# Kernel tuning notes

Measured on AMD Instinct MI355X. Metric: run time of the kernel, lower is better.

Reference implementation:

```python
import jax, jax.numpy as jnp
import numpy as np

N_EMBD = 1024
N_HEAD = 16
HEAD_DIM = N_EMBD // N_HEAD
INNER = 4 * N_EMBD
EPS = 1e-5


def setup_inputs() -> dict:
    key = jax.random.key(0)
    ks = jax.random.split(key, 13)
    s = lambda d: 1.0 / np.sqrt(d)
    return {
        "x": jax.random.normal(ks[0], (2, 2048, N_EMBD), jnp.float32),
        "ln1_g": jnp.ones((N_EMBD,), jnp.float32),
        "ln1_b": jnp.zeros((N_EMBD,), jnp.float32),
        "w_attn": jax.random.normal(ks[1], (N_EMBD, 3 * N_EMBD), jnp.float32) * s(N_EMBD),
        "b_attn": jnp.zeros((3 * N_EMBD,), jnp.float32),
        "w_proj": jax.random.normal(ks[2], (N_EMBD, N_EMBD), jnp.float32) * s(N_EMBD),
        "b_proj": jnp.zeros((N_EMBD,), jnp.float32),
        "ln2_g": jnp.ones((N_EMBD,), jnp.float32),
        "ln2_b": jnp.zeros((N_EMBD,), jnp.float32),
        "w_fc": jax.random.normal(ks[3], (N_EMBD, INNER), jnp.float32) * s(N_EMBD),
        "b_fc": jnp.zeros((INNER,), jnp.float32),
        "w_fc2": jax.random.normal(ks[4], (INNER, N_EMBD), jnp.float32) * s(INNER),
        "b_fc2": jnpp if False else jnp.zeros((N_EMBD,), jnp.float32),
    }


def _layernorm(x, g, b):
    mu = jnp.mean(x, axis=-1, keepdims=True)
    var = jnp.mean(jnp.square(x - mu), axis=-1, keepdims=True)
    return (x - mu) * jax.lax.rsqrt(var + EPS) * g + b


def _attention(x, w_attn, b_attn, w_proj, b_proj):
    B, T, C = x.shape
    qkv = x @ w_attn + b_attn                      # [B,T,3C]
    q, k, v = jnp.split(qkv, 3, axis=-1)
    q = q.reshape(B, T, N_HEAD, HEAD_DIM).transpose(0, 2, 1, 3)  # [B,H,T,D]
    k = k.reshape(B, T, N_HEAD, HEAD_DIM).transpose(0, 2, 1, 3)
    v = v.reshape(B, T, N_HEAD, HEAD_DIM).transpose(0, 2, 1, 3)
    scale = HEAD_DIM ** -0.5
    scores = jnp.einsum("bhqd,bhkd->bhqk", q, k) * scale         # [B,H,T,T]
    causal = jnp.triu(jnp.ones((T, T), jnp.bool_), k=1)
    scores = jnp.where(causal, -jnp.inf, scores)
    attn = jax.nn.softmax(scores, axis=-1)
    out = jnp.einsum("bhqk,bhkd->bhqd", attn, v)                 # [B,H,T,D]
    out = out.transpose(0, 2, 1, 3).reshape(B, T, C)
    return out @ w_proj + b_proj


def reference(x, ln1_g, ln1_b, w_attn, b_attn, w_proj, b_proj,
              ln2_g, ln2_b, w_fc, b_fc, w_fc2, b_fc2):
    h = x + _attention(_layernorm(x, ln1_g, ln1_b), w_attn, b_attn, w_proj, b_proj)
    m = _layernorm(h, ln2_g, ln2_b)
    m = jax.nn.gelu(m @ w_fc + b_fc, approximate=False) @ w_fc2 + b_fc2
    return h + m
```

## Files before the change

### kernel.cpp

```cpp
#include <hip/hip_runtime.h>

typedef unsigned short u16;
typedef unsigned int u32;
typedef short v8s __attribute__((ext_vector_type(8)));
typedef short v4s __attribute__((ext_vector_type(4)));
typedef float v4f __attribute__((ext_vector_type(4)));

__device__ __forceinline__ float b2f(u16 v) {
    return __uint_as_float(((u32)v) << 16);
}
__device__ __forceinline__ u16 f2b(float f) {
    u32 u = __float_as_uint(f);
    return (u16)((u + 0x7FFFu + ((u >> 16) & 1u)) >> 16);
}

__device__ __forceinline__ void gload_lds16(const u16* g, u16* l) {
    __builtin_amdgcn_global_load_lds((const __attribute__((address_space(1))) void*)g,
                                     (__attribute__((address_space(3))) void*)l, 16, 0, 0);
}

__global__ void detect_k(const void* x, int* flag) {
    __shared__ int cnt;
    if (threadIdx.x == 0) cnt = 0;
    __syncthreads();
    const u16* p = (const u16*)x;
    int bad = 0;
    for (int i = threadIdx.x; i < 4096; i += 256) {
        int e = (p[i] >> 7) & 0xFF;
        if (e != 0 && (e < 100 || e > 140)) bad++;
    }
    atomicAdd(&cnt, bad);
    __syncthreads();
    if (threadIdx.x == 0) *flag = (cnt > 256) ? 1 : 0;
}

__global__ void cvt_k(const void* __restrict__ src, u16* __restrict__ dst, int n,
                      const int* __restrict__ flag) {
    const int isf32 = *flag;
    for (int i = blockIdx.x * 256 + threadIdx.x; i < n; i += gridDim.x * 256)
        dst[i] = isf32 ? f2b(((const float*)src)[i]) : ((const u16*)src)[i];
}

struct P8 { const void* p[8]; };
__global__ void cvt_small_k(P8 src, u16* __restrict__ bb, const int* __restrict__ flag) {
    const int isf32 = *flag;
    const int len[8] = {3072, 1024, 4096, 1024, 1024, 1024, 1024, 1024};
    const int doff[8] = {0, 4096, 8192, 12288, 16384, 17408, 18432, 19456};
    int gi = blockIdx.x * 256 + threadIdx.x;
    int seg = 0, off = gi;
    while (seg < 7 && off >= len[seg]) { off -= len[seg]; seg++; }
    if (off < len[seg]) {
        const void* s = src.p[seg];
        bb[doff[seg] + off] = isf32 ? f2b(((const float*)s)[off]) : ((const u16*)s)[off];
    }
}

__global__ void transpose_k(const void* __restrict__ in, u16* __restrict__ out, int R, int C,
                            const int* __restrict__ flag) {
    __shared__ u16 t[32][33];
    const int isf32 = *flag;
    const int c0 = blockIdx.x * 32, r0 = blockIdx.y * 32;
    for (int i = threadIdx.y; i < 32; i += 8) {
        size_t idx = (size_t)(r0 + i) * C + c0 + threadIdx.x;
        t[i][threadIdx.x] = isf32 ? f2b(((const float*)in)[idx]) : ((const u16*)in)[idx];
    }
    __syncthreads();
    for (int i = threadIdx.y; i < 32; i += 8)
        out[(size_t)(c0 + i) * R + r0 + threadIdx.x] = t[threadIdx.x][i];
}

__global__ __launch_bounds__(256) void layernorm_k(const u16* __restrict__ x,
                                                   const u16* __restrict__ g,
                                                   const u16* __restrict__ bta,
                                                   u16* __restrict__ out) {
    const int wid = threadIdx.x >> 6, lane = threadIdx.x & 63;
    const size_t row = (size_t)blockIdx.x * 4 + wid;
    const u16* xr = x + row * 1024 + lane * 16;
    u16 v[16];
    *(uint4*)&v[0] = *(const uint4*)xr;
    *(uint4*)&v[8] = *(const uint4*)(xr + 8);
    float f[16], s = 0.f, sq = 0.f;
#pragma unroll
    for (int i = 0; i < 16; i++) { f[i] = b2f(v[i]); s += f[i]; sq += f[i] * f[i]; }
#pragma unroll
    for (int d = 1; d < 64; d <<= 1) { s += __shfl_xor(s, d, 64); sq += __shfl_xor(sq, d, 64); }
    const float mean = s * (1.f / 1024.f);
    const float var = sq * (1.f / 1024.f) - mean * mean;
    const float rstd = rsqrtf(var + 1e-5f);
    u16 gv[16], bv[16];
    *(uint4*)&gv[0] = *(const uint4*)(g + lane * 16);
    *(uint4*)&gv[8] = *(const uint4*)(g + lane * 16 + 8);
    *(uint4*)&bv[0] = *(const uint4*)(bta + lane * 16);
    *(uint4*)&bv[8] = *(const uint4*)(bta + lane * 16 + 8);
    u16 ov[16];
#pragma unroll
    for (int i = 0; i < 16; i++) ov[i] = f2b((f[i] - mean) * rstd * b2f(gv[i]) + b2f(bv[i]));
    u16* orow = out + row * 1024 + lane * 16;
    *(uint4*)orow = *(uint4*)&ov[0];
    *(uint4*)(orow + 8) = *(uint4*)&ov[8];
}

__global__ __launch_bounds__(256) void gemm_bt_k(const u16* __restrict__ A,
                                                 const u16* __restrict__ Bt,
                                                 const u16* __restrict__ bias,
                                                 const u16* __restrict__ res,
                                                 void* __restrict__ C,
                                                 int M, int N, int K, int do_gelu,
                                                 const int* __restrict__ outf32) {
    __shared__ __align__(16) u16 As[2][4096];
    __shared__ __align__(16) u16 Bs[2][4096];
    const int tid = threadIdx.x;
    const int wid = tid >> 6, lane = tid & 63;
    const int lg = lane >> 4, lm = lane & 15;
    const int wr = wid >> 1, wc = wid & 1;
    const int m0 = blockIdx.y * 128, n0 = blockIdx.x * 128;

    const v4f vzero = {0.f, 0.f, 0.f, 0.f};
    v4f acc[4][4];
#pragma unroll
    for (int i = 0; i < 4; i++)
#pragma unroll
        for (int j = 0; j < 4; j++) acc[i][j] = vzero;

    const int srow = tid >> 2;
    const int scol = (tid & 3) * 8;
    const u16* Ag = A + (size_t)(m0 + srow) * K + scol;
    const u16* Bg = Bt + (size_t)(n0 + srow) * K + scol;

    const int nt = K >> 5;
    {
        gload_lds16(Ag, &As[0][0] + wid * 512);
        gload_lds16(Ag + (size_t)64 * K, &As[0][2048] + wid * 512);
        gload_lds16(Bg, &Bs[0][0] + wid * 512);
        gload_lds16(Bg + (size_t)64 * K, &Bs[0][2048] + wid * 512);
    }
    for (int t = 0; t < nt; ++t) {
        const int cur = t & 1;
        if (t + 1 < nt) {
            const int k1 = (t + 1) << 5;
            gload_lds16(Ag + k1, &As[cur ^ 1][0] + wid * 512);
            gload_lds16(Ag + (size_t)64 * K + k1, &As[cur ^ 1][2048] + wid * 512);
            gload_lds16(Bg + k1, &Bs[cur ^ 1][0] + wid * 512);
            gload_lds16(Bg + (size_t)64 * K + k1, &Bs[cur ^ 1][2048] + wid * 512);
            asm volatile("s_waitcnt vmcnt(4)" ::: "memory");
        } else {
            asm volatile("s_waitcnt vmcnt(0)" ::: "memory");
        }
        __builtin_amdgcn_s_barrier();
        v8s af[4], bf[4];
#pragma unroll
        for (int i = 0; i < 4; i++)
            af[i] = *(const v8s*)&As[cur][(wr * 64 + i * 16 + lm) * 32 + lg * 8];
#pragma unroll
        for (int j = 0; j < 4; j++)
            bf[j] = *(const v8s*)&Bs[cur][(wc * 64 + j * 16 + lm) * 32 + lg * 8];
#pragma unroll
        for (int i = 0; i < 4; i++)
#pragma unroll
            for (int j = 0; j < 4; j++)
                acc[i][j] = __builtin_amdgcn_mfma_f32_16x16x32_bf16(af[i], bf[j], acc[i][j], 0, 0, 0);
        asm volatile("s_waitcnt lgkmcnt(0)" ::: "memory");
        __builtin_amdgcn_sched_barrier(0);
        __builtin_amdgcn_s_barrier();
    }

    const int of32 = outf32 ? *outf32 : 0;
#pragma unroll
    for (int i = 0; i < 4; i++) {
#pragma unroll
        for (int r = 0; r < 4; r++) {
            const int row = m0 + wr * 64 + i * 16 + lg * 4 + r;
            const size_t rb = (size_t)row * N;
#pragma unroll
            for (int j = 0; j < 4; j++) {
                const int col = n0 + wc * 64 + j * 16 + lm;
                float v = acc[i][j][r] + b2f(bias[col]);
                if (do_gelu) v = 0.5f * v * (1.0f + erff(v * 0.70710678118f));
                if (res) v += b2f(res[rb + col]);
                if (of32) ((float*)C)[rb + col] = v;
                else ((u16*)C)[rb + col] = f2b(v);
            }
        }
    }
}

__global__ __launch_bounds__(256) void gemm_qkv_k(const u16* __restrict__ A,
                                                  const u16* __restrict__ Bt,
                                                  const u16* __restrict__ bias,
                                                  u16* __restrict__ Qh,
                                                  u16* __restrict__ Kh,
                                                  u16* __restrict__ Vth) {
    __shared__ __align__(16) u16 As[2][4096];
    __shared__ __align__(16) u16 Bs[2][4096];
    const int tid = threadIdx.x;
    const int wid = tid >> 6, lane = tid & 63;
    const int lg = lane >> 4, lm = lane & 15;
    const int wr = wid >> 1, wc = wid & 1;
    const int m0 = blockIdx.y * 128, n0 = blockIdx.x * 128;
    const int K = 1024;

    const v4f vzero = {0.f, 0.f, 0.f, 0.f};
    v4f acc[4][4];
#pragma unroll
    for (int i = 0; i < 4; i++)
#pragma unroll
        for (int j = 0; j < 4; j++) acc[i][j] = vzero;

    const int srow = tid >> 2;
    const int scol = (tid & 3) * 8;
    const u16* Ag = A + (size_t)(m0 + srow) * K + scol;
    const u16* Bg = Bt + (size_t)(n0 + srow) * K + scol;

    const int nt = K >> 5;
    {
        gload_lds16(Ag, &As[0][0] + wid * 512);
        gload_lds16(Ag + (size_t)64 * K, &As[0][2048] + wid * 512);
        gload_lds16(Bg, &Bs[0][0] + wid * 512);
        gload_lds16(Bg + (size_t)64 * K, &Bs[0][2048] + wid * 512);
    }
    for (int t = 0; t < nt; ++t) {
        const int cur = t & 1;
        if (t + 1 < nt) {
            const int k1 = (t + 1) << 5;
            gload_lds16(Ag + k1, &As[cur ^ 1][0] + wid * 512);
            gload_lds16(Ag + (size_t)64 * K + k1, &As[cur ^ 1][2048] + wid * 512);
            gload_lds16(Bg + k1, &Bs[cur ^ 1][0] + wid * 512);
            gload_lds16(Bg + (size_t)64 * K + k1, &Bs[cur ^ 1][2048] + wid * 512);
            asm volatile("s_waitcnt vmcnt(4)" ::: "memory");
        } else {
            asm volatile("s_waitcnt vmcnt(0)" ::: "memory");
        }
        __builtin_amdgcn_s_barrier();
        v8s af[4], bf[4];
#pragma unroll
        for (int i = 0; i < 4; i++)
            af[i] = *(const v8s*)&As[cur][(wr * 64 + i * 16 + lm) * 32 + lg * 8];
#pragma unroll
        for (int j = 0; j < 4; j++)
            bf[j] = *(const v8s*)&Bs[cur][(wc * 64 + j * 16 + lm) * 32 + lg * 8];
#pragma unroll
        for (int i = 0; i < 4; i++)
#pragma unroll
            for (int j = 0; j < 4; j++)
                acc[i][j] = __builtin_amdgcn_mfma_f32_16x16x32_bf16(af[i], bf[j], acc[i][j], 0, 0, 0);
        asm volatile("s_waitcnt lgkmcnt(0)" ::: "memory");
        __builtin_amdgcn_sched_barrier(0);
        __builtin_amdgcn_s_barrier();
    }

    const int which = n0 >> 10;
    const int h = ((n0 & 1023) >> 6) + wc;
    if (which < 2) {
        u16* dst = which ? Kh : Qh;
        const float qsc = which ? 1.0f : 0.18033688011f;
#pragma unroll
        for (int i = 0; i < 4; i++) {
#pragma unroll
            for (int r = 0; r < 4; r++) {
                const int row = m0 + wr * 64 + i * 16 + lg * 4 + r;
                const int b = row >> 11, t = row & 2047;
                const size_t rb = ((size_t)(b * 16 + h) * 2048 + t) * 64;
#pragma unroll
                for (int j = 0; j < 4; j++) {
                    float v = (acc[i][j][r] + b2f(bias[n0 + wc * 64 + j * 16 + lm])) * qsc;
                    dst[rb + j * 16 + lm] = f2b(v);
                }
            }
        }
    } else {
#pragma unroll
        for (int i = 0; i < 4; i++) {
            const int t0 = m0 + wr * 64 + i * 16 + lg * 4;
            const int b = t0 >> 11, tt = t0 & 2047;
            const int w = tt & 31;
            const int pos = (tt & ~31) + ((w & 15) >> 2) * 8 + ((w >> 4) & 1) * 4;
#pragma unroll
            for (int j = 0; j < 4; j++) {
                const int d = j * 16 + lm;
                const float bv_ = b2f(bias[n0 + wc * 64 + j * 16 + lm]);
                u16 pk[4];
#pragma unroll
                for (int r = 0; r < 4; r++) pk[r] = f2b(acc[i][j][r] + bv_);
                *(v4s*)&Vth[((size_t)(b * 16 + h) * 64 + d) * 2048 + pos] = *(const v4s*)pk;
            }
        }
    }
}

__global__ __launch_bounds__(256, 4) void attn10_k(const u16* __restrict__ Qh,
                                                   const u16* __restrict__ Kh,
                                                   const u16* __restrict__ Vth,
                                                   u16* __restrict__ out) {
    __shared__ __align__(16) u16 Ks[2][4096];
    __shared__ __align__(16) u16 Vs[2][4096];
    const int tid = threadIdx.x;
    const int wid = tid >> 6, lane = tid & 63;
    const int lg = lane >> 4, lm = lane & 15;
    const int i = blockIdx.x;
    const int q = i >> 8, s = i & 255;
    const int bh = s & 31;
    const int g8 = s >> 5;
    const int g = (q == 0) ? g8 : (q == 1) ? (15 - g8) : (q == 2) ? (16 + g8) : (31 - g8);
    const int q0 = g * 64 + wid * 16;
    const int qrow_l = q0 + lm;
    const size_t qkb = (size_t)bh * 2048;
    const v4f vzero = {0.f, 0.f, 0.f, 0.f};
    const int nch = g + 1;

    const int r0 = tid >> 3;
    const int colp = ((tid & 7) * 16) ^ ((r0 & 7) << 4);
    const u16* Ksrc0 = Kh + (qkb + r0) * 64 + (colp >> 1);
    const u16* Ksrc1 = Ksrc0 + 32 * 64;
    const u16* Vsrc0 = Vth + ((size_t)bh * 64 + r0) * 2048 + (colp >> 1);
    const u16* Vsrc1 = Vsrc0 + (size_t)32 * 2048;
    const int wslot = wid * 512;

    const int xorv = (lm & 7) << 4;
    const int ro1 = (lm * 128 + ((lg * 16) ^ xorv)) >> 1;
    const int ro2 = (lm * 128 + (((lg * 16) + 64) ^ xorv)) >> 1;

    v8s aq[2];
    {
        const u16* qp = Qh + (qkb + q0 + lm) * 64 + lg * 8;
        aq[0] = *(const v8s*)qp;
        aq[1] = *(const v8s*)(qp + 32);
    }
    float l_run = 0.f;
    v4f o[4];
#pragma unroll
    for (int dt = 0; dt < 4; dt++) o[dt] = vzero;

    gload_lds16(Ksrc0, &Ks[0][0] + wslot);
    gload_lds16(Ksrc1, &Ks[0][2048] + wslot);
    gload_lds16(Vsrc0, &Vs[0][0] + wslot);
    gload_lds16(Vsrc1, &Vs[0][2048] + wslot);

    for (int ci = 0; ci < nch; ++ci) {
        const int cur = ci & 1;
        if (ci + 1 < nch) {
            const u16* kc = Ksrc0 + (ci + 1) * 4096;
            const u16* vc = Vsrc0 + (ci + 1) * 64;
            gload_lds16(kc, &Ks[cur ^ 1][0] + wslot);
            gload_lds16(kc + 32 * 64, &Ks[cur ^ 1][2048] + wslot);
            gload_lds16(vc, &Vs[cur ^ 1][0] + wslot);
            gload_lds16(vc + (size_t)32 * 2048, &Vs[cur ^ 1][2048] + wslot);
            asm volatile("s_waitcnt vmcnt(4)" ::: "memory");
        } else {
            asm volatile("s_waitcnt vmcnt(0)" ::: "memory");
        }
        __builtin_amdgcn_s_barrier();

        const u16* KB = &Ks[cur][0];
        const u16* VB = &Vs[cur][0];
        const int k0 = ci << 6;
        v4f sacc[4];
#pragma unroll
        for (int kt = 0; kt < 4; kt++) {
            v8s klo = *(const v8s*)(KB + kt * 1024 + ro1);
            v8s khi = *(const v8s*)(KB + kt * 1024 + ro2);
            sacc[kt] = __builtin_amdgcn_mfma_f32_16x16x32_bf16(klo, aq[0], vzero, 0, 0, 0);
            sacc[kt] = __builtin_amdgcn_mfma_f32_16x16x32_bf16(khi, aq[1], sacc[kt], 0, 0, 0);
        }
        float p[16];
        if (ci == nch - 1) {
#pragma unroll
            for (int kt = 0; kt < 4; kt++)
#pragma unroll
                for (int r = 0; r < 4; r++) {
                    float v = sacc[kt][r];
                    v = (k0 + kt * 16 + lg * 4 + r > qrow_l) ? -200.f : v;
                    p[kt * 4 + r] = exp2f(v);
                }
        } else {
#pragma unroll
            for (int kt = 0; kt < 4; kt++)
#pragma unroll
                for (int r = 0; r < 4; r++) p[kt * 4 + r] = exp2f(sacc[kt][r]);
        }
        float ls = 0.f;
#pragma unroll
        for (int e = 0; e < 16; e++) ls += p[e];
        l_run += ls;
        u32 pk[8];
#pragma unroll
        for (int j = 0; j < 8; j++) {
            u32 lo = __float_as_uint(p[j * 2]) + 0x8000u;
            u32 hi = __float_as_uint(p[j * 2 + 1]) + 0x8000u;
            pk[j] = __builtin_amdgcn_perm(hi, lo, 0x07060302u);
        }
        v8s B0, B1;
        ((u32*)&B0)[0] = pk[0]; ((u32*)&B0)[1] = pk[1];
        ((u32*)&B0)[2] = pk[2]; ((u32*)&B0)[3] = pk[3];
        ((u32*)&B1)[0] = pk[4]; ((u32*)&B1)[1] = pk[5];
        ((u32*)&B1)[2] = pk[6]; ((u32*)&B1)[3] = pk[7];
#pragma unroll
        for (int dt = 0; dt < 4; dt++) {
            v8s vlo = *(const v8s*)(VB + dt * 1024 + ro1);
            v8s vhi = *(const v8s*)(VB + dt * 1024 + ro2);
            o[dt] = __builtin_amdgcn_mfma_f32_16x16x32_bf16(vlo, B0, o[dt], 0, 0, 0);
            o[dt] = __builtin_amdgcn_mfma_f32_16x16x32_bf16(vhi, B1, o[dt], 0, 0, 0);
        }
        asm volatile("s_waitcnt lgkmcnt(0)" ::: "memory");
        __builtin_amdgcn_sched_barrier(0);
        __builtin_amdgcn_s_barrier();
    }
    l_run += __shfl_xor(l_run, 16, 64);
    l_run += __shfl_xor(l_run, 32, 64);
    const int b = bh >> 4, h = bh & 15;
    const float inv = 1.0f / l_run;
    const size_t rowb = ((size_t)b * 2048 + q0 + lm) * 1024 + h * 64;
#pragma unroll
    for (int dt = 0; dt < 4; dt++) {
        u16 pk2[4];
#pragma unroll
        for (int r = 0; r < 4; r++) pk2[r] = f2b(o[dt][r] * inv);
        *(v4s*)&out[rowb + dt * 16 + lg * 4] = *(const v4s*)pk2;
    }
}

extern "C" void kernel_launch(void* const* d_in, const int* in_sizes, int n_in,
                              void* d_out, int out_size, void* d_ws, size_t ws_size,
                              hipStream_t stream) {
    const void* x      = d_in[0];
    const void* ln1_g  = d_in[1];
    const void* ln1_b  = d_in[2];
    const void* w_attn = d_in[3];
    const void* b_attn = d_in[4];
    const void* w_proj = d_in[5];
    const void* b_proj = d_in[6];
    const void* ln2_g  = d_in[7];
    const void* ln2_b  = d_in[8];
    const void* w_fc   = d_in[9];
    const void* b_fc   = d_in[10];
    const void* w_fc2  = d_in[11];
    const void* b_fc2  = d_in[12];

    u16* ws = (u16*)d_ws;
    const size_t Mi = 1u << 20;
    u16* xb       = ws;
    u16* ln_buf   = ws + 4 * Mi;
    u16* h_buf    = ws + 8 * Mi;
    u16* wT_attn  = ws + 12 * Mi;
    u16* wT_proj  = ws + 15 * Mi;
    u16* wT_fc    = ws + 16 * Mi;
    u16* wT_fc2   = ws + 20 * Mi;
    u16* bb       = ws + 24 * Mi;
    u16* bb_attn = bb, *bb_proj = bb + 4096, *bb_fc = bb + 8192, *bb_fc2 = bb + 12288;
    u16* gsmall   = bb + 16384;
    u16* g_ln1g = gsmall, *g_ln1b = gsmall + 1024, *g_ln2g = gsmall + 2048, *g_ln2b = gsmall + 3072;
    int* flag     = (int*)(bb + 24576);
    u16* Qh       = ws + 25 * Mi;
    u16* Kh       = ws + 29 * Mi;
    u16* Vth      = ws + 33 * Mi;
    u16* attn_buf = ws + 37 * Mi;
    u16* fc_buf   = ws + 25 * Mi;

    detect_k<<<1, 256, 0, stream>>>(x, flag);

    cvt_k<<<4096, 256, 0, stream>>>(x, xb, 4 * Mi, flag);
    P8 smalls;
    smalls.p[0] = b_attn; smalls.p[1] = b_proj; smalls.p[2] = b_fc; smalls.p[3] = b_fc2;
    smalls.p[4] = ln1_g;  smalls.p[5] = ln1_b;  smalls.p[6] = ln2_g; smalls.p[7] = ln2_b;
    cvt_small_k<<<52, 256, 0, stream>>>(smalls, bb, flag);

    dim3 tb(32, 8);
    transpose_k<<<dim3(96, 32), tb, 0, stream>>>(w_attn, wT_attn, 1024, 3072, flag);
    transpose_k<<<dim3(32, 32), tb, 0, stream>>>(w_proj, wT_proj, 1024, 1024, flag);
    transpose_k<<<dim3(128, 32), tb, 0, stream>>>(w_fc, wT_fc, 1024, 4096, flag);
    transpose_k<<<dim3(32, 128), tb, 0, stream>>>(w_fc2, wT_fc2, 4096, 1024, flag);

    layernorm_k<<<1024, 256, 0, stream>>>(xb, g_ln1g, g_ln1b, ln_buf);
    gemm_qkv_k<<<dim3(24, 32), 256, 0, stream>>>(ln_buf, wT_attn, bb_attn, Qh, Kh, Vth);
    attn10_k<<<1024, 256, 0, stream>>>(Qh, Kh, Vth, attn_buf);
    gemm_bt_k<<<dim3(8, 32), 256, 0, stream>>>(attn_buf, wT_proj, bb_proj, xb, h_buf,
                                               4096, 1024, 1024, 0, nullptr);
    layernorm_k<<<1024, 256, 0, stream>>>(h_buf, g_ln2g, g_ln2b, ln_buf);
    gemm_bt_k<<<dim3(32, 32), 256, 0, stream>>>(ln_buf, wT_fc, bb_fc, nullptr, fc_buf,
                                                4096, 4096, 1024, 1, nullptr);
    gemm_bt_k<<<dim3(8, 32), 256, 0, stream>>>(fc_buf, wT_fc2, bb_fc2, h_buf, d_out,
                                               4096, 1024, 4096, 0, flag);
}
```

Measured before the change: 462.2 us.

## Triple-buffer GEMM loads, swizzle LDS, remap workgroups, raise MFMA priority

Moves both GEMM kernels from double to triple buffering, issuing loads two K-tiles ahead to hide more global latency. It also applies an XOR swizzle to the LDS layout to cut bank conflicts, remaps workgroup IDs in groups of 8 for better L2 locality, and wraps the MFMA sections of the GEMM and attention kernels in s_setprio. Costs are 1.5x LDS per block, which may lower occupancy, plus the assumption that the grid size divides evenly by 8.

```diff
diff --git a/kernel.cpp b/kernel.cpp
--- a/kernel.cpp
+++ b/kernel.cpp
@@ -100,6 +100,15 @@
     *(uint4*)(orow + 8) = *(uint4*)&ov[8];
 }
 
+#define GEMM_STAGE(tk, buf)                                              \
+    do {                                                                 \
+        const int _k = (tk) << 5;                                        \
+        gload_lds16(Ag + _k, &As[buf][0] + wid * 512);                   \
+        gload_lds16(Ag + (size_t)64 * K + _k, &As[buf][2048] + wid * 512); \
+        gload_lds16(Bg + _k, &Bs[buf][0] + wid * 512);                   \
+        gload_lds16(Bg + (size_t)64 * K + _k, &Bs[buf][2048] + wid * 512); \
+    } while (0)
+
 __global__ __launch_bounds__(256) void gemm_bt_k(const u16* __restrict__ A,
                                                  const u16* __restrict__ Bt,
                                                  const u16* __restrict__ bias,
@@ -107,13 +116,16 @@
                                                  void* __restrict__ C,
                                                  int M, int N, int K, int do_gelu,
                                                  const int* __restrict__ outf32) {
-    __shared__ __align__(16) u16 As[2][4096];
-    __shared__ __align__(16) u16 Bs[2][4096];
+    __shared__ __align__(16) u16 As[3][4096];
+    __shared__ __align__(16) u16 Bs[3][4096];
     const int tid = threadIdx.x;
     const int wid = tid >> 6, lane = tid & 63;
     const int lg = lane >> 4, lm = lane & 15;
     const int wr = wid >> 1, wc = wid & 1;
-    const int m0 = blockIdx.y * 128, n0 = blockIdx.x * 128;
+    const int nwg = gridDim.x * gridDim.y;
+    const int orig = blockIdx.y * gridDim.x + blockIdx.x;
+    const int wg = (orig & 7) * (nwg >> 3) + (orig >> 3);
+    const int m0 = (wg / gridDim.x) * 128, n0 = (wg % gridDim.x) * 128;
 
     const v4f vzero = {0.f, 0.f, 0.f, 0.f};
     v4f acc[4][4];
@@ -123,25 +135,20 @@
         for (int j = 0; j < 4; j++) acc[i][j] = vzero;
 
     const int srow = tid >> 2;
-    const int scol = (tid & 3) * 8;
+    const int scol = (((tid & 3) ^ ((tid >> 3) & 3)) * 8);
     const u16* Ag = A + (size_t)(m0 + srow) * K + scol;
     const u16* Bg = Bt + (size_t)(n0 + srow) * K + scol;
+    const int lgx = (lg ^ ((lm >> 1) & 3)) * 8;
 
     const int nt = K >> 5;
-    {
-        gload_lds16(Ag, &As[0][0] + wid * 512);
-        gload_lds16(Ag + (size_t)64 * K, &As[0][2048] + wid * 512);
-        gload_lds16(Bg, &Bs[0][0] + wid * 512);
-        gload_lds16(Bg + (size_t)64 * K, &Bs[0][2048] + wid * 512);
-    }
+    GEMM_STAGE(0, 0);
+    GEMM_STAGE(1, 1);
     for (int t = 0; t < nt; ++t) {
-        const int cur = t & 1;
-        if (t + 1 < nt) {
-            const int k1 = (t + 1) << 5;
-            gload_lds16(Ag + k1, &As[cur ^ 1][0] + wid * 512);
-            gload_lds16(Ag + (size_t)64 * K + k1, &As[cur ^ 1][2048] + wid * 512);
-            gload_lds16(Bg + k1, &Bs[cur ^ 1][0] + wid * 512);
-            gload_lds16(Bg + (size_t)64 * K + k1, &Bs[cur ^ 1][2048] + wid * 512);
+        const int cur = t % 3;
+        if (t + 2 < nt) {
+            GEMM_STAGE(t + 2, (t + 2) % 3);
+            asm volatile("s_waitcnt vmcnt(8)" ::: "memory");
+        } else if (t + 1 < nt) {
             asm volatile("s_waitcnt vmcnt(4)" ::: "memory");
         } else {
             asm volatile("s_waitcnt vmcnt(0)" ::: "memory");
@@ -150,15 +157,17 @@
         v8s af[4], bf[4];
 #pragma unroll
         for (int i = 0; i < 4; i++)
-            af[i] = *(const v8s*)&As[cur][(wr * 64 + i * 16 + lm) * 32 + lg * 8];
+            af[i] = *(const v8s*)&As[cur][(wr * 64 + i * 16 + lm) * 32 + lgx];
 #pragma unroll
         for (int j = 0; j < 4; j++)
-            bf[j] = *(const v8s*)&Bs[cur][(wc * 64 + j * 16 + lm) * 32 + lg * 8];
+            bf[j] = *(const v8s*)&Bs[cur][(wc * 64 + j * 16 + lm) * 32 + lgx];
+        __builtin_amdgcn_s_setprio(1);
 #pragma unroll
         for (int i = 0; i < 4; i++)
 #pragma unroll
             for (int j = 0; j < 4; j++)
                 acc[i][j] = __builtin_amdgcn_mfma_f32_16x16x32_bf16(af[i], bf[j], acc[i][j], 0, 0, 0);
+        __builtin_amdgcn_s_setprio(0);
         asm volatile("s_waitcnt lgkmcnt(0)" ::: "memory");
         __builtin_amdgcn_sched_barrier(0);
         __builtin_amdgcn_s_barrier();
@@ -190,13 +199,16 @@
                                                   u16* __restrict__ Qh,
                                                   u16* __restrict__ Kh,
                                                   u16* __restrict__ Vth) {
-    __shared__ __align__(16) u16 As[2][4096];
-    __shared__ __align__(16) u16 Bs[2][4096];
+    __shared__ __align__(16) u16 As[3][4096];
+    __shared__ __align__(16) u16 Bs[3][4096];
     const int tid = threadIdx.x;
     const int wid = tid >> 6, lane = tid & 63;
     const int lg = lane >> 4, lm = lane & 15;
     const int wr = wid >> 1, wc = wid & 1;
-    const int m0 = blockIdx.y * 128, n0 = blockIdx.x * 128;
+    const int nwg = gridDim.x * gridDim.y;
+    const int orig = blockIdx.y * gridDim.x + blockIdx.x;
+    const int wg = (orig & 7) * (nwg >> 3) + (orig >> 3);
+    const int m0 = (wg / gridDim.x) * 128, n0 = (wg % gridDim.x) * 128;
     const int K = 1024;
 
     const v4f vzero = {0.f, 0.f, 0.f, 0.f};
@@ -207,25 +219,20 @@
         for (int j = 0; j < 4; j++) acc[i][j] = vzero;
 
     const int srow = tid >> 2;
-    const int scol = (tid & 3) * 8;
+    const int scol = (((tid & 3) ^ ((tid >> 3) & 3)) * 8);
     const u16* Ag = A + (size_t)(m0 + srow) * K + scol;
     const u16* Bg = Bt + (size_t)(n0 + srow) * K + scol;
+    const int lgx = (lg ^ ((lm >> 1) & 3)) * 8;
 
     const int nt = K >> 5;
-    {
-        gload_lds16(Ag, &As[0][0] + wid * 512);
-        gload_lds16(Ag + (size_t)64 * K, &As[0][2048] + wid * 512);
-        gload_lds16(Bg, &Bs[0][0] + wid * 512);
-        gload_lds16(Bg + (size_t)64 * K, &Bs[0][2048] + wid * 512);
-    }
+    GEMM_STAGE(0, 0);
+    GEMM_STAGE(1, 1);
     for (int t = 0; t < nt; ++t) {
-        const int cur = t & 1;
-        if (t + 1 < nt) {
-            const int k1 = (t + 1) << 5;
-            gload_lds16(Ag + k1, &As[cur ^ 1][0] + wid * 512);
-            gload_lds16(Ag + (size_t)64 * K + k1, &As[cur ^ 1][2048] + wid * 512);
-            gload_lds16(Bg + k1, &Bs[cur ^ 1][0] + wid * 512);
-            gload_lds16(Bg + (size_t)64 * K + k1, &Bs[cur ^ 1][2048] + wid * 512);
+        const int cur = t % 3;
+        if (t + 2 < nt) {
+            GEMM_STAGE(t + 2, (t + 2) % 3);
+            asm volatile("s_waitcnt vmcnt(8)" ::: "memory");
+        } else if (t + 1 < nt) {
             asm volatile("s_waitcnt vmcnt(4)" ::: "memory");
         } else {
             asm volatile("s_waitcnt vmcnt(0)" ::: "memory");
@@ -234,15 +241,17 @@
         v8s af[4], bf[4];
 #pragma unroll
         for (int i = 0; i < 4; i++)
-            af[i] = *(const v8s*)&As[cur][(wr * 64 + i * 16 + lm) * 32 + lg * 8];
+            af[i] = *(const v8s*)&As[cur][(wr * 64 + i * 16 + lm) * 32 + lgx];
 #pragma unroll
         for (int j = 0; j < 4; j++)
-            bf[j] = *(const v8s*)&Bs[cur][(wc * 64 + j * 16 + lm) * 32 + lg * 8];
+            bf[j] = *(const v8s*)&Bs[cur][(wc * 64 + j * 16 + lm) * 32 + lgx];
+        __builtin_amdgcn_s_setprio(1);
 #pragma unroll
         for (int i = 0; i < 4; i++)
 #pragma unroll
             for (int j = 0; j < 4; j++)
                 acc[i][j] = __builtin_amdgcn_mfma_f32_16x16x32_bf16(af[i], bf[j], acc[i][j], 0, 0, 0);
+        __builtin_amdgcn_s_setprio(0);
         asm volatile("s_waitcnt lgkmcnt(0)" ::: "memory");
         __builtin_amdgcn_sched_barrier(0);
         __builtin_amdgcn_s_barrier();
@@ -354,6 +363,7 @@
         const u16* VB = &Vs[cur][0];
         const int k0 = ci << 6;
         v4f sacc[4];
+        __builtin_amdgcn_s_setprio(1);
 #pragma unroll
         for (int kt = 0; kt < 4; kt++) {
             v8s klo = *(const v8s*)(KB + kt * 1024 + ro1);
@@ -361,6 +371,7 @@
             sacc[kt] = __builtin_amdgcn_mfma_f32_16x16x32_bf16(klo, aq[0], vzero, 0, 0, 0);
             sacc[kt] = __builtin_amdgcn_mfma_f32_16x16x32_bf16(khi, aq[1], sacc[kt], 0, 0, 0);
         }
+        __builtin_amdgcn_s_setprio(0);
         float p[16];
         if (ci == nch - 1) {
 #pragma unroll
@@ -393,6 +404,7 @@
         ((u32*)&B0)[2] = pk[2]; ((u32*)&B0)[3] = pk[3];
         ((u32*)&B1)[0] = pk[4]; ((u32*)&B1)[1] = pk[5];
         ((u32*)&B1)[2] = pk[6]; ((u32*)&B1)[3] = pk[7];
+        __builtin_amdgcn_s_setprio(1);
 #pragma unroll
         for (int dt = 0; dt < 4; dt++) {
             v8s vlo = *(const v8s*)(VB + dt * 1024 + ro1);
@@ -400,6 +412,7 @@
             o[dt] = __builtin_amdgcn_mfma_f32_16x16x32_bf16(vlo, B0, o[dt], 0, 0, 0);
             o[dt] = __builtin_amdgcn_mfma_f32_16x16x32_bf16(vhi, B1, o[dt], 0, 0, 0);
         }
+        __builtin_amdgcn_s_setprio(0);
         asm volatile("s_waitcnt lgkmcnt(0)" ::: "memory");
         __builtin_amdgcn_sched_barrier(0);
         __builtin_amdgcn_s_barrier();
```

New measurement: 455.2 us. About the same (-1.5%).
